# Performance work log

Measured on AMD Instinct MI355X. Metric: run time of the kernel, lower is better.

The kernel has to match this reference:

```python
import jax, jax.numpy as jnp
import numpy as np

N = 100000      # nodes
E = 1600000     # edges (avg degree 16)
NFEAT = 128
NHID = 128
LRELU_SLOPE = 0.2

def setup_inputs() -> dict:
    key = jax.random.key(0)
    ks = jax.random.split(key, 12)
    s = 1.0 / np.sqrt(NFEAT)
    inp = {}
    inp["x"] = jax.random.normal(ks[0], (N, NFEAT), dtype=jnp.float32)
    inp["edge_row"] = jax.random.randint(ks[1], (E,), 0, N, dtype=jnp.int32)
    inp["edge_col"] = jax.random.randint(ks[2], (E,), 0, N, dtype=jnp.int32)
    inp["edge_val"] = jax.random.uniform(ks[3], (E,), dtype=jnp.float32)
    inp["norm"] = jax.random.uniform(ks[4], (N, 1), dtype=jnp.float32) * 16.0 + 1.0
    # Relation params (bias-free Linears, torch layout y = x @ W.T)
    inp["Wg1"] = jax.random.uniform(ks[5], (NFEAT, NFEAT), minval=-s, maxval=s, dtype=jnp.float32)
    inp["Wg2"] = jax.random.uniform(ks[6], (NFEAT, NFEAT), minval=-s, maxval=s, dtype=jnp.float32)
    inp["Wb1"] = jax.random.uniform(ks[7], (NFEAT, NFEAT), minval=-s, maxval=s, dtype=jnp.float32)
    inp["Wb2"] = jax.random.uniform(ks[8], (NFEAT, NFEAT), minval=-s, maxval=s, dtype=jnp.float32)
    inp["r"] = jax.random.uniform(ks[9], (1, NFEAT), minval=-s, maxval=s, dtype=jnp.float32)
    # GraphConv weight [nfeat, nhid]
    inp["gc_w"] = jax.random.uniform(ks[10], (NFEAT, NHID), minval=-s, maxval=s, dtype=jnp.float32)
    return inp

def _spmm(edge_row, edge_col, edge_val, h):
    # sparse [N,N] @ dense [N,D] via gather + segment-sum
    return jax.ops.segment_sum(edge_val[:, None] * h[edge_col], edge_row, num_segments=N)

def reference(x, edge_row, edge_col, edge_val, norm, Wg1, Wg2, Wb1, Wb2, r, gc_w):
    # neighbor = sp.mm(adj, x)
    neighbor = _spmm(edge_row, edge_col, edge_val, x)
    # Relation (ver=1, ablation=0): FiLM-modulated transE relation vector
    gamma = jax.nn.leaky_relu(x @ Wg1.T + neighbor @ Wg2.T, LRELU_SLOPE) + 1.0
    beta = jax.nn.leaky_relu(x @ Wb1.T + neighbor @ Wb2.T, LRELU_SLOPE)
    m = x + (gamma * r + beta) - neighbor
    # tail branch (head=False, ablation=0): h_s = m @ gc.weight
    h_s = m @ gc_w
    # GraphConv with adj_self = adj + I (no norm inside)
    xw = x @ gc_w
    h_k = _spmm(edge_row, edge_col, edge_val, xw) + xw
    h_k = (h_k + h_s) / (norm + 1.0)
    return (h_k, m)
```

## Files before the change

kernel.cpp:

```cpp
#include <hip/hip_runtime.h>

#define N_NODES 100000
#define NFEAT 128
#define E_EDGES 1600000
#define LRELU_SLOPE 0.2f
#define BM 32
#define NB2 3125
#define SCAP 2048
#define SC_BLOCKS 128
#define SC_PER 12500
#define XB_BLOCKS 3125
#define PK_BLOCKS 320

typedef short bf16x8 __attribute__((ext_vector_type(8)));
typedef float f32x4 __attribute__((ext_vector_type(4)));

__device__ __forceinline__ ushort f2bf(float f) {
    union { float f; uint u; } v; v.f = f;
    uint u = v.u;
    return (ushort)((u + 0x7fffu + ((u >> 16) & 1u)) >> 16);
}
__device__ __forceinline__ float bf2f(ushort s) {
    union { uint u; float f; } v; v.u = ((uint)s) << 16;
    return v.f;
}
__device__ __forceinline__ float blo(uint u) {
    union { uint u; float f; } v; v.u = u << 16; return v.f;
}
__device__ __forceinline__ float bhi(uint u) {
    union { uint u; float f; } v; v.u = u & 0xFFFF0000u; return v.f;
}

__global__ __launch_bounds__(256) void mega_prep(
    const int* __restrict__ er, const int* __restrict__ ec,
    const float* __restrict__ ev, int* __restrict__ cursorB,
    int2* __restrict__ stg,
    const float* __restrict__ x, ushort* __restrict__ xb,
    const float* __restrict__ Wg1, const float* __restrict__ Wg2,
    const float* __restrict__ Wb1, const float* __restrict__ Wb2,
    const float* __restrict__ gcw,
    ushort* __restrict__ W1p, ushort* __restrict__ W2p)
{
    __shared__ int harr[NB2];
    const int bid = blockIdx.x;
    const int tid = threadIdx.x;

    if (bid < SC_BLOCKS) {
        const int e0 = bid * SC_PER, e1 = e0 + SC_PER;
        for (int k = tid; k < NB2; k += 256) harr[k] = 0;
        __syncthreads();
        for (int e = e0 + tid; e < e1; e += 256) atomicAdd(&harr[er[e] >> 5], 1);
        __syncthreads();
        for (int k = tid; k < NB2; k += 256) {
            int h = harr[k];
            if (h) harr[k] = (k * SCAP + atomicAdd(&cursorB[k], h)) << 8;
        }
        __syncthreads();
        for (int e = e0 + tid; e < e1; e += 256) {
            int r = er[e];
            int t = atomicAdd(&harr[r >> 5], 1);
            int2 o;
            o.x = (ec[e] << 13) | (r & 31);
            o.y = __float_as_int(ev[e]);
            stg[(t >> 8) + (t & 255)] = o;
        }
    } else if (bid < SC_BLOCKS + XB_BLOCKS) {
        size_t base = ((size_t)(bid - SC_BLOCKS) * 256 + tid) * 16;
        float4 a = *reinterpret_cast<const float4*>(x + base);
        float4 b = *reinterpret_cast<const float4*>(x + base + 4);
        float4 c = *reinterpret_cast<const float4*>(x + base + 8);
        float4 d = *reinterpret_cast<const float4*>(x + base + 12);
        uint4 o1, o2;
        o1.x = (uint)f2bf(a.x) | ((uint)f2bf(a.y) << 16);
        o1.y = (uint)f2bf(a.z) | ((uint)f2bf(a.w) << 16);
        o1.z = (uint)f2bf(b.x) | ((uint)f2bf(b.y) << 16);
        o1.w = (uint)f2bf(b.z) | ((uint)f2bf(b.w) << 16);
        o2.x = (uint)f2bf(c.x) | ((uint)f2bf(c.y) << 16);
        o2.y = (uint)f2bf(c.z) | ((uint)f2bf(c.w) << 16);
        o2.z = (uint)f2bf(d.x) | ((uint)f2bf(d.y) << 16);
        o2.w = (uint)f2bf(d.z) | ((uint)f2bf(d.w) << 16);
        *reinterpret_cast<uint4*>(xb + base) = o1;
        *reinterpret_cast<uint4*>(xb + base + 8) = o2;
    } else {
        int idx = (bid - SC_BLOCKS - XB_BLOCKS) * 256 + tid;
        if (idx < 65536) {
            int jj = idx & 7;
            int lane = (idx >> 3) & 63;
            int tile = idx >> 9;
            int nt = tile & 15, kt = tile >> 4;
            int k = kt * 32 + (lane >> 4) * 8 + jj;
            int j = nt * 16 + (lane & 15);
            float v;
            if (j < 128) v = (k < 128) ? Wg1[j * 128 + k] : Wg2[j * 128 + (k - 128)];
            else { int c = j - 128; v = (k < 128) ? Wb1[c * 128 + k] : Wb2[c * 128 + (k - 128)]; }
            W1p[idx] = f2bf(v);
        } else if (idx < 81920) {
            int i2 = idx - 65536;
            int jj = i2 & 7;
            int lane = (i2 >> 3) & 63;
            int tile = i2 >> 9;
            int nt = tile & 7, kt = tile >> 3;
            int k = kt * 32 + (lane >> 4) * 8 + jj;
            int j = nt * 16 + (lane & 15);
            W2p[i2] = f2bf(gcw[k * 128 + j]);
        }
    }
}

__global__ __launch_bounds__(512, 8) void fused_all(
    const int* __restrict__ cursorB, const int2* stg,
    const ushort* __restrict__ xb,
    const float* __restrict__ norm, const float* __restrict__ rvec,
    const ushort* __restrict__ W1p, const ushort* __restrict__ W2p,
    float* hk, float* __restrict__ mout)
{
    __shared__ ushort SM[16384];
    __shared__ int h32[32], rs32[32], pd32[32], cur32[32];
    char* asb = (char*)SM;
    char* gbb = (char*)(SM + 8192);
    int2* elist = (int2*)gbb;

    const int tid = threadIdx.x;
    const int lane = tid & 63;
    const int w = tid >> 6;
    const int g = lane >> 4;
    const int s = lane & 15;
    const int b = blockIdx.x;
    const int node0 = b * BM;

    {
        int rr = tid >> 4;
        int cq = tid & 15;
        uint4 v = *reinterpret_cast<const uint4*>(xb + (size_t)(node0 + rr) * 128 + cq * 8);
        *(uint4*)(asb + ((rr * 512 + cq * 16) ^ ((rr & 7) << 4))) = v;
    }

    const int cntE = cursorB[b];
    const int2* sb = stg + (size_t)b * SCAP;
    int2 E0, E1;
    const bool v0 = tid < cntE, v1 = tid + 512 < cntE;
    if (v0) E0 = sb[tid];
    if (v1) E1 = sb[tid + 512];
    if (tid < 32) h32[tid] = 0;
    __syncthreads();
    if (v0) atomicAdd(&h32[E0.x & 31], 1);
    if (v1) atomicAdd(&h32[E1.x & 31], 1);
    __syncthreads();
    if (tid < 64) {
        int pc = 0;
        if (tid < 32) { int h = h32[tid]; pc = (h + 7) & ~7; cur32[tid] = 0; }
        int v = pc;
        for (int off = 1; off < 32; off <<= 1) {
            int t = __shfl_up(v, off, 64);
            if (lane >= off) v += t;
        }
        if (tid < 32) { rs32[tid] = v - pc; pd32[tid] = pc; }
    }
    __syncthreads();
    if (v0) { int rl = E0.x & 31; elist[rs32[rl] + atomicAdd(&cur32[rl], 1)] = E0; }
    if (v1) { int rl = E1.x & 31; elist[rs32[rl] + atomicAdd(&cur32[rl], 1)] = E1; }
    if (tid < 32) {
        int rs = rs32[tid];
        for (int j = h32[tid]; j < pd32[tid]; ++j) elist[rs + j] = make_int2(tid, 0);
    }
    __syncthreads();

    const char* xbase = (const char*)xb + s * 16;
#pragma unroll 1
    for (int i = 0; i < 4; i++) {
        int rr = w * 4 + i;
        const int2* el = elist + rs32[rr];
        int pd = pd32[rr];
        float ac0 = 0.f, ac1 = 0.f, ac2 = 0.f, ac3 = 0.f;
        float ac4 = 0.f, ac5 = 0.f, ac6 = 0.f, ac7 = 0.f;
#pragma unroll 2
        for (int j = 0; j < pd; j += 8) {
            int2 e0 = el[j + g];
            int2 e1 = el[j + 4 + g];
            uint4 q0 = *reinterpret_cast<const uint4*>(xbase + (e0.x >> 5));
            uint4 q1 = *reinterpret_cast<const uint4*>(xbase + (e1.x >> 5));
            float f0 = __int_as_float(e0.y);
            float f1 = __int_as_float(e1.y);
            ac0 += f0 * blo(q0.x); ac1 += f0 * bhi(q0.x);
            ac2 += f0 * blo(q0.y); ac3 += f0 * bhi(q0.y);
            ac4 += f0 * blo(q0.z); ac5 += f0 * bhi(q0.z);
            ac6 += f0 * blo(q0.w); ac7 += f0 * bhi(q0.w);
            ac0 += f1 * blo(q1.x); ac1 += f1 * bhi(q1.x);
            ac2 += f1 * blo(q1.y); ac3 += f1 * bhi(q1.y);
            ac4 += f1 * blo(q1.z); ac5 += f1 * bhi(q1.z);
            ac6 += f1 * blo(q1.w); ac7 += f1 * bhi(q1.w);
        }
        ac0 += __shfl_xor(ac0, 16, 64); ac0 += __shfl_xor(ac0, 32, 64);
        ac1 += __shfl_xor(ac1, 16, 64); ac1 += __shfl_xor(ac1, 32, 64);
        ac2 += __shfl_xor(ac2, 16, 64); ac2 += __shfl_xor(ac2, 32, 64);
        ac3 += __shfl_xor(ac3, 16, 64); ac3 += __shfl_xor(ac3, 32, 64);
        ac4 += __shfl_xor(ac4, 16, 64); ac4 += __shfl_xor(ac4, 32, 64);
        ac5 += __shfl_xor(ac5, 16, 64); ac5 += __shfl_xor(ac5, 32, 64);
        ac6 += __shfl_xor(ac6, 16, 64); ac6 += __shfl_xor(ac6, 32, 64);
        ac7 += __shfl_xor(ac7, 16, 64); ac7 += __shfl_xor(ac7, 32, 64);
        if (g == 0) {
            uint4 o;
            o.x = (uint)f2bf(ac0) | ((uint)f2bf(ac1) << 16);
            o.y = (uint)f2bf(ac2) | ((uint)f2bf(ac3) << 16);
            o.z = (uint)f2bf(ac4) | ((uint)f2bf(ac5) << 16);
            o.w = (uint)f2bf(ac6) | ((uint)f2bf(ac7) << 16);
            *(uint4*)(asb + ((rr * 512 + 256 + s * 16) ^ ((rr & 7) << 4))) = o;
        }
    }
    __syncthreads();

    f32x4 acc[2][2];
#pragma unroll
    for (int mt = 0; mt < 2; mt++)
#pragma unroll
        for (int nl = 0; nl < 2; nl++) acc[mt][nl] = (f32x4){0.f, 0.f, 0.f, 0.f};

#pragma unroll
    for (int kt = 0; kt < 8; kt++) {
        bf16x8 af[2];
#pragma unroll
        for (int mt = 0; mt < 2; mt++) {
            int row = mt * 16 + (lane & 15);
            int off = (row * 512 + kt * 64 + (lane >> 4) * 16) ^ ((row & 7) << 4);
            af[mt] = *(bf16x8*)(asb + off);
        }
#pragma unroll
        for (int nl = 0; nl < 2; nl++) {
            int nt = w * 2 + nl;
            bf16x8 bfg = *(const bf16x8*)(W1p + (((kt * 16 + nt) * 64 + lane) << 3));
#pragma unroll
            for (int mt = 0; mt < 2; mt++)
                acc[mt][nl] = __builtin_amdgcn_mfma_f32_16x16x32_bf16(af[mt], bfg, acc[mt][nl], 0, 0, 0);
        }
    }

#pragma unroll
    for (int mt = 0; mt < 2; mt++)
#pragma unroll
        for (int nl = 0; nl < 2; nl++) {
            int j = (w * 2 + nl) * 16 + (lane & 15);
#pragma unroll
            for (int reg = 0; reg < 4; reg++) {
                int row = mt * 16 + (lane >> 4) * 4 + reg;
                int off = (row * 512 + j * 2) ^ ((row & 7) << 4);
                *(ushort*)(gbb + off) = f2bf(acc[mt][nl][reg]);
            }
        }
    __syncthreads();

    {
        int c = tid & 127;
        float rv = rvec[c];
        int rg = tid >> 7;
#pragma unroll 4
        for (int i = 0; i < 8; i++) {
            int row = rg * 8 + i;
            int swz = (row & 7) << 4;
            int bx = (row * 512 + c * 2) ^ swz;
            int bn = (row * 512 + 256 + c * 2) ^ swz;
            float graw = bf2f(*(ushort*)(gbb + bx));
            float braw = bf2f(*(ushort*)(gbb + bn));
            float xv = bf2f(*(ushort*)(asb + bx));
            float nv = bf2f(*(ushort*)(asb + bn));
            float gamma = ((graw > 0.f) ? graw : LRELU_SLOPE * graw) + 1.f;
            float beta = (braw > 0.f) ? braw : LRELU_SLOPE * braw;
            float gb_ = gamma * rv + beta;
            float mv = xv + gb_ - nv;
            float tv = 2.f * xv + gb_;
            mout[(size_t)(node0 + row) * 128 + c] = mv;
            *(ushort*)(asb + bx) = f2bf(tv);
        }
    }
    __syncthreads();

    f32x4 acc2[2];
#pragma unroll
    for (int mt = 0; mt < 2; mt++) acc2[mt] = (f32x4){0.f, 0.f, 0.f, 0.f};

#pragma unroll
    for (int kt = 0; kt < 4; kt++) {
        bf16x8 af[2];
#pragma unroll
        for (int mt = 0; mt < 2; mt++) {
            int row = mt * 16 + (lane & 15);
            int off = (row * 512 + kt * 64 + (lane >> 4) * 16) ^ ((row & 7) << 4);
            af[mt] = *(bf16x8*)(asb + off);
        }
        bf16x8 bfg = *(const bf16x8*)(W2p + (((kt * 8 + w) * 64 + lane) << 3));
#pragma unroll
        for (int mt = 0; mt < 2; mt++)
            acc2[mt] = __builtin_amdgcn_mfma_f32_16x16x32_bf16(af[mt], bfg, acc2[mt], 0, 0, 0);
    }

#pragma unroll
    for (int mt = 0; mt < 2; mt++) {
        int col = w * 16 + (lane & 15);
#pragma unroll
        for (int reg = 0; reg < 4; reg++) {
            int row = mt * 16 + (lane >> 4) * 4 + reg;
            int node = node0 + row;
            float inv = 1.f / (norm[node] + 1.f);
            hk[(size_t)node * 128 + col] = acc2[mt][reg] * inv;
        }
    }
}

extern "C" void kernel_launch(void* const* d_in, const int* in_sizes, int n_in,
                              void* d_out, int out_size, void* d_ws, size_t ws_size,
                              hipStream_t stream)
{
    const float* x    = (const float*)d_in[0];
    const int*   er   = (const int*)d_in[1];
    const int*   ec   = (const int*)d_in[2];
    const float* ev   = (const float*)d_in[3];
    const float* norm = (const float*)d_in[4];
    const float* Wg1  = (const float*)d_in[5];
    const float* Wg2  = (const float*)d_in[6];
    const float* Wb1  = (const float*)d_in[7];
    const float* Wb2  = (const float*)d_in[8];
    const float* r    = (const float*)d_in[9];
    const float* gcw  = (const float*)d_in[10];

    float* out  = (float*)d_out;
    float* hk   = out;
    float* mout = out + (size_t)N_NODES * NFEAT;

    ushort* xb      = (ushort*)d_ws;
    ushort* W1p     = xb + (size_t)N_NODES * NFEAT;
    ushort* W2p     = W1p + 65536;
    int*    cursorB = (int*)(W2p + 16384);

    int2* stg = (int2*)hk;

    hipMemsetAsync(cursorB, 0, NB2 * sizeof(int), stream);

    mega_prep<<<SC_BLOCKS + XB_BLOCKS + PK_BLOCKS, 256, 0, stream>>>(
        er, ec, ev, cursorB, stg, x, xb,
        Wg1, Wg2, Wb1, Wb2, gcw, W1p, W2p);

    fused_all<<<NB2, 512, 0, stream>>>(
        cursorB, stg, xb, norm, r, W1p, W2p, hk, mout);
}
```

Baseline: 163.0 us.

## Split edge bucketing into histogram, scan and scatter kernels

Replaces the single-pass bucketing, which claimed space with global atomics per block and bucket, with a three-phase counting sort. Per-block histograms are written to workspace, a scan kernel computes deterministic per-block offsets and bucket counts, and a separate scatter kernel places the edges. This removes global atomic contention and the memset, and gives contiguous per-block placement. In exchange it adds two kernel launches, a serial 256-step scan per bucket, and extra workspace traffic for the histograms.

```diff
diff --git a/kernel.cpp b/kernel.cpp
--- a/kernel.cpp
+++ b/kernel.cpp
@@ -7,8 +7,8 @@
 #define BM 32
 #define NB2 3125
 #define SCAP 2048
-#define SC_BLOCKS 128
-#define SC_PER 12500
+#define HB_BLOCKS 256
+#define HB_PER 6250
 #define XB_BLOCKS 3125
 #define PK_BLOCKS 320
 
@@ -32,40 +32,27 @@
 }
 
 __global__ __launch_bounds__(256) void mega_prep(
-    const int* __restrict__ er, const int* __restrict__ ec,
-    const float* __restrict__ ev, int* __restrict__ cursorB,
-    int2* __restrict__ stg,
+    const int* __restrict__ er, int* __restrict__ ghist,
     const float* __restrict__ x, ushort* __restrict__ xb,
     const float* __restrict__ Wg1, const float* __restrict__ Wg2,
     const float* __restrict__ Wb1, const float* __restrict__ Wb2,
     const float* __restrict__ gcw,
     ushort* __restrict__ W1p, ushort* __restrict__ W2p)
 {
-    __shared__ int harr[NB2];
+    __shared__ int hist[NB2];
     const int bid = blockIdx.x;
     const int tid = threadIdx.x;
 
-    if (bid < SC_BLOCKS) {
-        const int e0 = bid * SC_PER, e1 = e0 + SC_PER;
-        for (int k = tid; k < NB2; k += 256) harr[k] = 0;
+    if (bid < HB_BLOCKS) {
+        for (int k = tid; k < NB2; k += 256) hist[k] = 0;
         __syncthreads();
-        for (int e = e0 + tid; e < e1; e += 256) atomicAdd(&harr[er[e] >> 5], 1);
+        const int e0 = bid * HB_PER;
+        for (int k = tid; k < HB_PER; k += 256)
+            atomicAdd(&hist[er[e0 + k] >> 5], 1);
         __syncthreads();
-        for (int k = tid; k < NB2; k += 256) {
-            int h = harr[k];
-            if (h) harr[k] = (k * SCAP + atomicAdd(&cursorB[k], h)) << 8;
-        }
-        __syncthreads();
-        for (int e = e0 + tid; e < e1; e += 256) {
-            int r = er[e];
-            int t = atomicAdd(&harr[r >> 5], 1);
-            int2 o;
-            o.x = (ec[e] << 13) | (r & 31);
-            o.y = __float_as_int(ev[e]);
-            stg[(t >> 8) + (t & 255)] = o;
-        }
-    } else if (bid < SC_BLOCKS + XB_BLOCKS) {
-        size_t base = ((size_t)(bid - SC_BLOCKS) * 256 + tid) * 16;
+        for (int k = tid; k < NB2; k += 256) ghist[bid * NB2 + k] = hist[k];
+    } else if (bid < HB_BLOCKS + XB_BLOCKS) {
+        size_t base = ((size_t)(bid - HB_BLOCKS) * 256 + tid) * 16;
         float4 a = *reinterpret_cast<const float4*>(x + base);
         float4 b = *reinterpret_cast<const float4*>(x + base + 4);
         float4 c = *reinterpret_cast<const float4*>(x + base + 8);
@@ -82,7 +69,7 @@
         *reinterpret_cast<uint4*>(xb + base) = o1;
         *reinterpret_cast<uint4*>(xb + base + 8) = o2;
     } else {
-        int idx = (bid - SC_BLOCKS - XB_BLOCKS) * 256 + tid;
+        int idx = (bid - HB_BLOCKS - XB_BLOCKS) * 256 + tid;
         if (idx < 65536) {
             int jj = idx & 7;
             int lane = (idx >> 3) & 63;
@@ -104,6 +91,44 @@
             int j = nt * 16 + (lane & 15);
             W2p[i2] = f2bf(gcw[k * 128 + j]);
         }
+    }
+}
+
+__global__ __launch_bounds__(256) void scan_hist(
+    const int* __restrict__ ghist, int* __restrict__ gbase,
+    int* __restrict__ cursorB)
+{
+    int c = blockIdx.x * 256 + threadIdx.x;
+    if (c >= NB2) return;
+    int acc = c * SCAP;
+#pragma unroll 8
+    for (int r = 0; r < HB_BLOCKS; r++) {
+        gbase[r * NB2 + c] = acc;
+        acc += ghist[r * NB2 + c];
+    }
+    cursorB[c] = acc - c * SCAP;
+}
+
+__global__ __launch_bounds__(512) void scatter_edges(
+    const int* __restrict__ er, const int* __restrict__ ec,
+    const float* __restrict__ ev, const int* __restrict__ gbase,
+    int2* __restrict__ stg)
+{
+    __shared__ int cur[NB2];
+    const int bid = blockIdx.x;
+    const int tid = threadIdx.x;
+    for (int k = tid; k < NB2; k += 512) cur[k] = gbase[bid * NB2 + k];
+    __syncthreads();
+    const int e0 = bid * HB_PER;
+#pragma unroll 2
+    for (int k = tid; k < HB_PER; k += 512) {
+        int e = e0 + k;
+        int r = er[e];
+        int t = atomicAdd(&cur[r >> 5], 1);
+        int2 o;
+        o.x = (ec[e] << 13) | (r & 31);
+        o.y = __float_as_int(ev[e]);
+        stg[t] = o;
     }
 }
 
@@ -329,14 +354,17 @@
     ushort* W1p     = xb + (size_t)N_NODES * NFEAT;
     ushort* W2p     = W1p + 65536;
     int*    cursorB = (int*)(W2p + 16384);
+    int*    ghist   = cursorB + NB2;
+    int*    gbase   = ghist + HB_BLOCKS * NB2;
 
     int2* stg = (int2*)hk;
 
-    hipMemsetAsync(cursorB, 0, NB2 * sizeof(int), stream);
-
-    mega_prep<<<SC_BLOCKS + XB_BLOCKS + PK_BLOCKS, 256, 0, stream>>>(
-        er, ec, ev, cursorB, stg, x, xb,
-        Wg1, Wg2, Wb1, Wb2, gcw, W1p, W2p);
+    mega_prep<<<HB_BLOCKS + XB_BLOCKS + PK_BLOCKS, 256, 0, stream>>>(
+        er, ghist, x, xb, Wg1, Wg2, Wb1, Wb2, gcw, W1p, W2p);
+
+    scan_hist<<<(NB2 + 255) / 256, 256, 0, stream>>>(ghist, gbase, cursorB);
+
+    scatter_edges<<<HB_BLOCKS, 512, 0, stream>>>(er, ec, ev, gbase, stg);
 
     fused_all<<<NB2, 512, 0, stream>>>(
         cursorB, stg, xb, norm, r, W1p, W2p, hk, mout);
```

Result: faster. 155.4 us (-4.7%).
